# Optimization experiments

Hardware: AMD Instinct MI355X
Metric: run time of the kernel (lower is better)

## Reference

```python
import jax, jax.numpy as jnp
import numpy as np

B, T, E, H = 2, 2048, 1024, 16
D = E // H  # head_dim = 64


def setup_inputs() -> dict:
    key = jax.random.key(0)
    ks = jax.random.split(key, 9)
    s = 0.02
    x = jax.random.normal(ks[0], (B, T, E), dtype=jnp.float32)
    # additive causal mask, broadcastable to (B, H, T, T)
    causal = jnp.tril(jnp.ones((T, T), dtype=bool))
    uni_causal_mask = jnp.where(causal, 0.0, -1e9).astype(jnp.float32)[None, None]
    # torch Linear weights are (out_features, in_features); out = H*D, in = D
    Wq = jax.random.normal(ks[1], (H * D, D), dtype=jnp.float32) * s
    bq = jax.random.normal(ks[2], (H * D,), dtype=jnp.float32) * s
    Wk = jax.random.normal(ks[3], (H * D, D), dtype=jnp.float32) * s
    bk = jax.random.normal(ks[4], (H * D,), dtype=jnp.float32) * s
    Wv = jax.random.normal(ks[5], (H * D, D), dtype=jnp.float32) * s
    bv = jax.random.normal(ks[6], (H * D,), dtype=jnp.float32) * s
    Wp = jax.random.normal(ks[7], (E, E), dtype=jnp.float32) * s
    bp = jax.random.normal(ks[8], (E,), dtype=jnp.float32) * s
    return {"x": x, "uni_causal_mask": uni_causal_mask,
            "Wq": Wq, "bq": bq, "Wk": Wk, "bk": bk,
            "Wv": Wv, "bv": bv, "Wp": Wp, "bp": bp}


def _per_head_proj(xh, W, b):
    # xh: (B, T, H, D). Original code projects each head's D-dim slice with
    # Linear(D, H*D) and get_head_dim keeps only the diagonal block i for
    # head i, i.e. each head uses W[i*D:(i+1)*D, :] and b[i*D:(i+1)*D].
    W3 = W.reshape(H, D, D)  # (H, out D, in D)
    b2 = b.reshape(H, D)
    y = jnp.einsum('bthi,hoi->bhto', xh, W3) + b2[None, :, None, :]
    return y  # (B, H, T, D)


def reference(x, uni_causal_mask, Wq, bq, Wk, bk, Wv, bv, Wp, bp):
    b, t, e = x.shape
    xh = x.reshape(b, t, H, D)
    q = _per_head_proj(xh, Wq, bq)  # (B,H,T,D)
    k = _per_head_proj(xh, Wk, bk)
    v = _per_head_proj(xh, Wv, bv)
    scale = D ** (-0.5)
    attn = jnp.einsum('bhtd,bhsd->bhts', (q * scale).astype(jnp.float32),
                      k.astype(jnp.float32))
    attn = attn + uni_causal_mask
    attn = jax.nn.softmax(attn, axis=-1).astype(x.dtype)
    out = jnp.einsum('bhts,bhsd->bhtd', attn, v)
    out = out.transpose(0, 2, 1, 3).reshape(b, t, e)
    return out @ Wp.T + bp
```

## Files before the change

kernel.cpp:

```cpp
#include <hip/hip_runtime.h>

typedef __attribute__((ext_vector_type(4))) float f32x4;
typedef __attribute__((ext_vector_type(8))) __bf16 bf16x8;
typedef __attribute__((ext_vector_type(4))) unsigned short us4;
typedef __attribute__((ext_vector_type(8))) unsigned short us8;

#define DEVI static __device__ __forceinline__

constexpr int T_ = 2048, E_ = 1024, H_ = 16, D_ = 64;
#define QSCALE (0.125f * 1.44269504088896f)

DEVI unsigned short f2b(float f) {
  union { float fv; unsigned u; } c; c.fv = f;
  unsigned r = c.u + 0x7fffu + ((c.u >> 16) & 1u);
  return (unsigned short)(r >> 16);
}

#if __has_builtin(__builtin_amdgcn_exp2f)
DEVI float fexp2(float x) { return __builtin_amdgcn_exp2f(x); }
#else
DEVI float fexp2(float x) { return __expf(x * 0.69314718056f); }
#endif

DEVI f32x4 mfma16(bf16x8 a, bf16x8 b, f32x4 c) {
  return __builtin_amdgcn_mfma_f32_16x16x32_bf16(a, b, c, 0, 0, 0);
}

__launch_bounds__(256)
__global__ void wcvt_kernel(const float* __restrict__ Wq,
                            const float* __restrict__ Wk,
                            const float* __restrict__ Wv,
                            unsigned short* __restrict__ wqb,
                            unsigned short* __restrict__ wkb,
                            unsigned short* __restrict__ wvb)
{
  int blk = blockIdx.x;
  const float* src; unsigned short* dst; float s = 1.0f;
  if (blk < 64)       { src = Wq; dst = wqb; s = QSCALE; }
  else if (blk < 128) { src = Wk; dst = wkb; blk -= 64; }
  else                { src = Wv; dst = wvb; blk -= 128; }
  int i = blk * 256 + threadIdx.x;
  float4 v = *(const float4*)(src + (size_t)i * 4);
  us4 o; o[0] = f2b(v.x * s); o[1] = f2b(v.y * s); o[2] = f2b(v.z * s); o[3] = f2b(v.w * s);
  *(us4*)(dst + (size_t)i * 4) = o;
}

__launch_bounds__(256)
__global__ void wpcvt_kernel(const float* __restrict__ Wp,
                             unsigned short* __restrict__ wpb)
{
  int i = blockIdx.x * 256 + threadIdx.x;
  float4 v = *(const float4*)(Wp + (size_t)i * 4);
  us4 o; o[0] = f2b(v.x); o[1] = f2b(v.y); o[2] = f2b(v.z); o[3] = f2b(v.w);
  *(us4*)(wpb + (size_t)i * 4) = o;
}

__launch_bounds__(256)
__global__ void qkv_kernel(const float* __restrict__ x,
                           const unsigned short* __restrict__ wqb,
                           const float* __restrict__ bq,
                           const unsigned short* __restrict__ wkb,
                           const float* __restrict__ bk,
                           const unsigned short* __restrict__ wvb,
                           const float* __restrict__ bv,
                           unsigned short* __restrict__ qo,
                           unsigned short* __restrict__ ko,
                           unsigned short* __restrict__ vto)
{
  const int bh = blockIdx.x;
  const int b  = bh >> 4;
  const int h  = bh & (H_ - 1);
  const int t0 = blockIdx.y * 128;
  __shared__ unsigned short Xl[128][72];
  __shared__ unsigned short Wl[3][64][72];
  const int tid = threadIdx.x;

  #pragma unroll
  for (int p = 0; p < 8; ++p) {
    int idx = p * 256 + tid;
    int row = idx >> 4, c4 = idx & 15;
    const float* gp = x + ((size_t)(b * T_ + t0 + row)) * E_ + h * 64 + c4 * 4;
    float4 v = *(const float4*)gp;
    us4 o; o[0] = f2b(v.x); o[1] = f2b(v.y); o[2] = f2b(v.z); o[3] = f2b(v.w);
    *(us4*)&Xl[row][c4 * 4] = o;
  }
  {
    const unsigned short* wsrc0 = wqb + (size_t)h * 4096;
    const unsigned short* wsrc1 = wkb + (size_t)h * 4096;
    const unsigned short* wsrc2 = wvb + (size_t)h * 4096;
    #pragma unroll
    for (int p = 0; p < 2; ++p) {
      int idx = p * 256 + tid;
      int row = idx >> 3, c8 = (idx & 7) * 8;
      *(us8*)&Wl[0][row][c8] = *(const us8*)(wsrc0 + row * 64 + c8);
      *(us8*)&Wl[1][row][c8] = *(const us8*)(wsrc1 + row * 64 + c8);
      *(us8*)&Wl[2][row][c8] = *(const us8*)(wsrc2 + row * 64 + c8);
    }
  }
  __syncthreads();

  const int w = tid >> 6, lane = tid & 63, lo = lane & 15, g = lane >> 4;
  const int tl0 = w * 32;

  bf16x8 xb[2][2];
  #pragma unroll
  for (int tt = 0; tt < 2; ++tt)
    #pragma unroll
    for (int kd = 0; kd < 2; ++kd)
      xb[tt][kd] = *(const bf16x8*)&Xl[tl0 + tt * 16 + lo][kd * 32 + g * 8];

  #pragma unroll
  for (int tsel = 0; tsel < 2; ++tsel) {
    const float* bias = tsel ? bk : bq;
    unsigned short* outp = tsel ? ko : qo;
    const float bs = tsel ? 1.0f : QSCALE;
    #pragma unroll
    for (int ot = 0; ot < 4; ++ot) {
      bf16x8 a0 = *(const bf16x8*)&Wl[tsel][ot * 16 + lo][g * 8];
      bf16x8 a1 = *(const bf16x8*)&Wl[tsel][ot * 16 + lo][32 + g * 8];
      float4 bv4 = *(const float4*)(bias + h * 64 + ot * 16 + g * 4);
      float bb[4] = {bv4.x * bs, bv4.y * bs, bv4.z * bs, bv4.w * bs};
      #pragma unroll
      for (int tt = 0; tt < 2; ++tt) {
        f32x4 acc = {0.f, 0.f, 0.f, 0.f};
        acc = mfma16(a0, xb[tt][0], acc);
        acc = mfma16(a1, xb[tt][1], acc);
        int tg = t0 + tl0 + tt * 16 + lo;
        us4 pk;
        #pragma unroll
        for (int r = 0; r < 4; ++r) pk[r] = f2b(acc[r] + bb[r]);
        *(us4*)(outp + ((size_t)(bh * T_ + tg)) * 64 + ot * 16 + g * 4) = pk;
      }
    }
  }

  #pragma unroll
  for (int rt = 0; rt < 2; ++rt) {
    bf16x8 a0 = *(const bf16x8*)&Xl[tl0 + rt * 16 + lo][g * 8];
    bf16x8 a1 = *(const bf16x8*)&Xl[tl0 + rt * 16 + lo][32 + g * 8];
    #pragma unroll
    for (int ct = 0; ct < 4; ++ct) {
      bf16x8 b0 = *(const bf16x8*)&Wl[2][ct * 16 + lo][g * 8];
      bf16x8 b1 = *(const bf16x8*)&Wl[2][ct * 16 + lo][32 + g * 8];
      f32x4 acc = {0.f, 0.f, 0.f, 0.f};
      acc = mfma16(a0, b0, acc);
      acc = mfma16(a1, b1, acc);
      int d = ct * 16 + lo;
      float bvs = bv[h * 64 + d];
      int tg = t0 + tl0 + rt * 16 + g * 4;
      us4 pk;
      #pragma unroll
      for (int r = 0; r < 4; ++r) pk[r] = f2b(acc[r] + bvs);
      *(us4*)(vto + ((size_t)(bh * 64 + d)) * T_ + tg) = pk;
    }
  }
}

__launch_bounds__(256)
__global__ void flash_kernel(const unsigned short* __restrict__ q,
                             const unsigned short* __restrict__ kk_,
                             const unsigned short* __restrict__ vt,
                             unsigned short* __restrict__ ao)
{
  const int bh = blockIdx.x;
  const int b = bh >> 4, h = bh & 15;
  __shared__ unsigned short Kl[2][64][64];
  __shared__ unsigned short Vl[2][64][64];
  __shared__ unsigned short Pl[4][16][64];
  const int tid = threadIdx.x, w = tid >> 6, lane = tid & 63, lo = lane & 15, g = lane >> 4;
  const int rs = lo & 7;

  const int srow = tid >> 3, sgi = tid & 7;
  const int sgis = (sgi ^ (srow & 7)) * 8;
  const unsigned short* kbase = kk_ + ((size_t)bh * T_ + srow) * 64 + sgi * 8;
  const unsigned short* vbase = vt + ((size_t)(bh * 64 + srow)) * T_ + sgi * 8;

  #pragma unroll 1
  for (int half = 0; half < 2; ++half) {
    const int qt = half ? (31 - blockIdx.y) : blockIdx.y;
    const int t0 = qt * 64;
    const int tw = t0 + w * 16;

    bf16x8 qf[2];
    const unsigned short* qb = q + ((size_t)(bh * T_ + tw + lo)) * 64;
    #pragma unroll
    for (int kd = 0; kd < 2; ++kd)
      qf[kd] = *(const bf16x8*)(qb + kd * 32 + g * 8);

    float m_ = -1e30f, l_ = 0.f;
    f32x4 zero4 = {0.f, 0.f, 0.f, 0.f};
    f32x4 oacc[4];
    #pragma unroll
    for (int dt = 0; dt < 4; ++dt) oacc[dt] = zero4;

    const int nsteps = qt + 1;
    us8 kr0 = *(const us8*)(kbase);
    us8 kr1 = *(const us8*)(kbase + 2048);
    us8 vr0 = *(const us8*)(vbase);
    us8 vr1 = *(const us8*)(vbase + (size_t)32 * T_);
    *(us8*)&Kl[0][srow][sgis] = kr0;
    *(us8*)&Kl[0][srow + 32][sgis] = kr1;
    *(us8*)&Vl[0][srow][sgis] = vr0;
    *(us8*)&Vl[0][srow + 32][sgis] = vr1;
    if (nsteps > 1) {
      kr0 = *(const us8*)(kbase + 4096);
      kr1 = *(const us8*)(kbase + 4096 + 2048);
      vr0 = *(const us8*)(vbase + 64);
      vr1 = *(const us8*)(vbase + 64 + (size_t)32 * T_);
    }
    __syncthreads();

    for (int stp = 0; stp < nsteps; ++stp) {
      const int s0 = stp * 64;
      const int cur = stp & 1;
      us8 nk0, nk1, nv0, nv1;
      const bool pf = (stp + 2 < nsteps);
      if (pf) {
        const size_t ko_ = (size_t)(stp + 2) * 4096;
        nk0 = *(const us8*)(kbase + ko_);
        nk1 = *(const us8*)(kbase + ko_ + 2048);
        nv0 = *(const us8*)(vbase + (stp + 2) * 64);
        nv1 = *(const us8*)(vbase + (stp + 2) * 64 + (size_t)32 * T_);
      }
      {
        f32x4 sacc[4];
        #pragma unroll
        for (int ss = 0; ss < 4; ++ss) sacc[ss] = zero4;
        __builtin_amdgcn_s_setprio(1);
        #pragma unroll
        for (int ss = 0; ss < 4; ++ss) {
          bf16x8 ka0 = *(const bf16x8*)&Kl[cur][ss * 16 + lo][(g ^ rs) * 8];
          bf16x8 ka1 = *(const bf16x8*)&Kl[cur][ss * 16 + lo][((g | 4) ^ rs) * 8];
          sacc[ss] = mfma16(ka0, qf[0], sacc[ss]);
          sacc[ss] = mfma16(ka1, qf[1], sacc[ss]);
        }
        __builtin_amdgcn_s_setprio(0);
        if (s0 + 63 > tw) {
          #pragma unroll
          for (int ss = 0; ss < 4; ++ss)
            #pragma unroll
            for (int r = 0; r < 4; ++r) {
              int sg = s0 + ss * 16 + g * 4 + r;
              if (sg > tw + lo) sacc[ss][r] = -1e30f;
            }
        }
        float mx = -1e30f;
        #pragma unroll
        for (int ss = 0; ss < 4; ++ss)
          #pragma unroll
          for (int r = 0; r < 4; ++r) mx = fmaxf(mx, sacc[ss][r]);
        mx = fmaxf(mx, __shfl_xor(mx, 16));
        mx = fmaxf(mx, __shfl_xor(mx, 32));
        float mn = fmaxf(m_, mx);
        float corr = fexp2(m_ - mn);
        m_ = mn;
        float sum = 0.f;
        #pragma unroll
        for (int ss = 0; ss < 4; ++ss) {
          us4 pk;
          #pragma unroll
          for (int r = 0; r < 4; ++r) {
            float pv = fexp2(sacc[ss][r] - mn);
            sum += pv;
            pk[r] = f2b(pv);
          }
          *(us4*)&Pl[w][lo][(((ss * 2 + (g >> 1)) ^ rs) << 3) + (g & 1) * 4] = pk;
        }
        sum += __shfl_xor(sum, 16);
        sum += __shfl_xor(sum, 32);
        l_ = l_ * corr + sum;
        #pragma unroll
        for (int dt = 0; dt < 4; ++dt) oacc[dt] *= corr;
        __builtin_amdgcn_s_setprio(1);
        #pragma unroll
        for (int kh = 0; kh < 2; ++kh) {
          bf16x8 pb = *(const bf16x8*)&Pl[w][lo][((kh * 4 + g) ^ rs) * 8];
          #pragma unroll
          for (int dt = 0; dt < 4; ++dt) {
            bf16x8 va = *(const bf16x8*)&Vl[cur][dt * 16 + lo][((kh * 4 + g) ^ rs) * 8];
            oacc[dt] = mfma16(va, pb, oacc[dt]);
          }
        }
        __builtin_amdgcn_s_setprio(0);
      }
      if (stp + 1 < nsteps) {
        *(us8*)&Kl[cur ^ 1][srow][sgis] = kr0;
        *(us8*)&Kl[cur ^ 1][srow + 32][sgis] = kr1;
        *(us8*)&Vl[cur ^ 1][srow][sgis] = vr0;
        *(us8*)&Vl[cur ^ 1][srow + 32][sgis] = vr1;
      }
      __syncthreads();
      if (pf) { kr0 = nk0; kr1 = nk1; vr0 = nv0; vr1 = nv1; }
    }
    float inv = 1.0f / l_;
    unsigned short* op = ao + ((size_t)(b * T_ + tw + lo)) * E_ + h * 64;
    #pragma unroll
    for (int dt = 0; dt < 4; ++dt) {
      us4 pk;
      #pragma unroll
      for (int r = 0; r < 4; ++r) pk[r] = f2b(oacc[dt][r] * inv);
      *(us4*)(op + dt * 16 + g * 4) = pk;
    }
  }
}

__launch_bounds__(256)
__global__ void proj_kernel(const unsigned short* __restrict__ ao,
                            const unsigned short* __restrict__ wpb,
                            const float* __restrict__ bp,
                            float* __restrict__ out)
{
  const int m0 = blockIdx.x * 128;
  const int n0 = blockIdx.y * 64;
  __shared__ unsigned short Al[2][128][40];
  __shared__ unsigned short Bl[2][64][40];
  const int tid = threadIdx.x, w = tid >> 6, lane = tid & 63, lo = lane & 15, g = lane >> 4;
  const int wr = (w >> 1) * 64, wc = (w & 1) * 32;
  f32x4 zero4 = {0.f, 0.f, 0.f, 0.f};
  f32x4 acc[4][2];
  #pragma unroll
  for (int i = 0; i < 4; ++i)
    #pragma unroll
    for (int j = 0; j < 2; ++j) acc[i][j] = zero4;

  const int arow = tid >> 1, acol = (tid & 1) * 16;
  const int brow = tid >> 2, bcol = (tid & 3) * 8;
  const unsigned short* abase = ao + (size_t)(m0 + arow) * 1024 + acol;
  const unsigned short* bbase = wpb + (size_t)(n0 + brow) * 1024 + bcol;

  us8 a0 = *(const us8*)(abase);
  us8 a1 = *(const us8*)(abase + 8);
  us8 b0 = *(const us8*)(bbase);
  *(us8*)&Al[0][arow][acol] = a0;
  *(us8*)&Al[0][arow][acol + 8] = a1;
  *(us8*)&Bl[0][brow][bcol] = b0;
  a0 = *(const us8*)(abase + 32);
  a1 = *(const us8*)(abase + 40);
  b0 = *(const us8*)(bbase + 32);
  __syncthreads();

  for (int it = 0; it < 32; ++it) {
    const int cur = it & 1;
    us8 na0, na1, nb0;
    const bool pf = (it + 2 < 32);
    if (pf) {
      const int kn = (it + 2) * 32;
      na0 = *(const us8*)(abase + kn);
      na1 = *(const us8*)(abase + kn + 8);
      nb0 = *(const us8*)(bbase + kn);
    }
    bf16x8 af[4], bfr[2];
    #pragma unroll
    for (int i = 0; i < 4; ++i) af[i] = *(const bf16x8*)&Al[cur][wr + i * 16 + lo][g * 8];
    #pragma unroll
    for (int j = 0; j < 2; ++j) bfr[j] = *(const bf16x8*)&Bl[cur][wc + j * 16 + lo][g * 8];
    __builtin_amdgcn_s_setprio(1);
    #pragma unroll
    for (int i = 0; i < 4; ++i)
      #pragma unroll
      for (int j = 0; j < 2; ++j)
        acc[i][j] = mfma16(af[i], bfr[j], acc[i][j]);
    __builtin_amdgcn_s_setprio(0);
    if (it + 1 < 32) {
      *(us8*)&Al[cur ^ 1][arow][acol] = a0;
      *(us8*)&Al[cur ^ 1][arow][acol + 8] = a1;
      *(us8*)&Bl[cur ^ 1][brow][bcol] = b0;
    }
    __syncthreads();
    if (pf) { a0 = na0; a1 = na1; b0 = nb0; }
  }
  #pragma unroll
  for (int j = 0; j < 2; ++j) {
    int n = n0 + wc + j * 16 + lo;
    float bias = bp[n];
    #pragma unroll
    for (int i = 0; i < 4; ++i) {
      #pragma unroll
      for (int r = 0; r < 4; ++r)
        out[(size_t)(m0 + wr + i * 16 + g * 4 + r) * 1024 + n] = acc[i][j][r] + bias;
    }
  }
}

extern "C" void kernel_launch(void* const* d_in, const int* in_sizes, int n_in,
                              void* d_out, int out_size, void* d_ws, size_t ws_size,
                              hipStream_t stream)
{
  const float* x  = (const float*)d_in[0];
  const float* Wq = (const float*)d_in[2];
  const float* bq = (const float*)d_in[3];
  const float* Wk = (const float*)d_in[4];
  const float* bk = (const float*)d_in[5];
  const float* Wv = (const float*)d_in[6];
  const float* bv = (const float*)d_in[7];
  const float* Wp = (const float*)d_in[8];
  const float* bp = (const float*)d_in[9];
  float* out = (float*)d_out;

  char* ws = (char*)d_ws;
  const size_t SZ = (size_t)2 * 16 * 2048 * 64 * 2;
  unsigned short* q  = (unsigned short*)(ws);
  unsigned short* kb = (unsigned short*)(ws + SZ);
  unsigned short* vt = (unsigned short*)(ws + 2 * SZ);
  unsigned short* ao = (unsigned short*)(ws + 3 * SZ);
  unsigned short* wqb = ao;
  unsigned short* wkb = ao + 65536;
  unsigned short* wvb = ao + 131072;
  unsigned short* wpb = q;

  wcvt_kernel<<<dim3(192), 256, 0, stream>>>(Wq, Wk, Wv, wqb, wkb, wvb);
  qkv_kernel<<<dim3(32, 16), 256, 0, stream>>>(x, wqb, bq, wkb, bk, wvb, bv, q, kb, vt);
  flash_kernel<<<dim3(32, 16), 256, 0, stream>>>(q, kb, vt, ao);
  wpcvt_kernel<<<dim3(1024), 256, 0, stream>>>(Wp, wpb);
  proj_kernel<<<dim3(32, 16), 256, 0, stream>>>(ao, wpb, bp, out);
}
```

Measured before the change: 89.05 us.

## Restructure flash attention to 128-row query tiles with async LDS loads and lazy rescale

The flash kernel now gives each block one 128-row query tile, with every wave handling 32 rows. Each K/V tile loaded into LDS is therefore reused across twice as many query rows. Causal load balance is kept by pairing tiles through the blockIdx.y mapping. Register-staged K/V prefetch is replaced with direct global-to-LDS loads. The online-softmax rescale is skipped when the new row max exceeds the old by no more than 8, which keeps the output exact but lets the exp values grow larger. Separately, the QKV kernel moves to 64-row tiles with twice as many blocks, and the bf16 conversion uses the native cast. The costs are higher register pressure and a wave-uniform early-exit on the causal tile loop.

```diff
diff --git a/kernel.cpp b/kernel.cpp
--- a/kernel.cpp
+++ b/kernel.cpp
@@ -11,9 +11,7 @@
 #define QSCALE (0.125f * 1.44269504088896f)
 
 DEVI unsigned short f2b(float f) {
-  union { float fv; unsigned u; } c; c.fv = f;
-  unsigned r = c.u + 0x7fffu + ((c.u >> 16) & 1u);
-  return (unsigned short)(r >> 16);
+  union { __bf16 b; unsigned short u; } c; c.b = (__bf16)f; return c.u;
 }
 
 #if __has_builtin(__builtin_amdgcn_exp2f)
@@ -24,6 +22,12 @@
 
 DEVI f32x4 mfma16(bf16x8 a, bf16x8 b, f32x4 c) {
   return __builtin_amdgcn_mfma_f32_16x16x32_bf16(a, b, c, 0, 0, 0);
+}
+
+DEVI void gl16(const void* g, void* l) {
+  __builtin_amdgcn_global_load_lds(
+      (const __attribute__((address_space(1))) unsigned int*)g,
+      (__attribute__((address_space(3))) unsigned int*)l, 16, 0, 0);
 }
 
 __launch_bounds__(256)
@@ -70,17 +74,16 @@
   const int bh = blockIdx.x;
   const int b  = bh >> 4;
   const int h  = bh & (H_ - 1);
-  const int t0 = blockIdx.y * 128;
-  __shared__ unsigned short Xl[128][72];
+  const int t0 = blockIdx.y * 64;
+  __shared__ unsigned short Xl[64][72];
   __shared__ unsigned short Wl[3][64][72];
   const int tid = threadIdx.x;
 
   #pragma unroll
-  for (int p = 0; p < 8; ++p) {
+  for (int p = 0; p < 4; ++p) {
     int idx = p * 256 + tid;
     int row = idx >> 4, c4 = idx & 15;
-    const float* gp = x + ((size_t)(b * T_ + t0 + row)) * E_ + h * 64 + c4 * 4;
-    float4 v = *(const float4*)gp;
+    float4 v = *(const float4*)(x + ((size_t)(b * T_ + t0 + row)) * E_ + h * 64 + c4 * 4);
     us4 o; o[0] = f2b(v.x); o[1] = f2b(v.y); o[2] = f2b(v.z); o[3] = f2b(v.w);
     *(us4*)&Xl[row][c4 * 4] = o;
   }
@@ -100,14 +103,12 @@
   __syncthreads();
 
   const int w = tid >> 6, lane = tid & 63, lo = lane & 15, g = lane >> 4;
-  const int tl0 = w * 32;
-
-  bf16x8 xb[2][2];
-  #pragma unroll
-  for (int tt = 0; tt < 2; ++tt)
-    #pragma unroll
-    for (int kd = 0; kd < 2; ++kd)
-      xb[tt][kd] = *(const bf16x8*)&Xl[tl0 + tt * 16 + lo][kd * 32 + g * 8];
+  const int tl0 = w * 16;
+
+  bf16x8 xb[2];
+  #pragma unroll
+  for (int kd = 0; kd < 2; ++kd)
+    xb[kd] = *(const bf16x8*)&Xl[tl0 + lo][kd * 32 + g * 8];
 
   #pragma unroll
   for (int tsel = 0; tsel < 2; ++tsel) {
@@ -119,25 +120,20 @@
       bf16x8 a0 = *(const bf16x8*)&Wl[tsel][ot * 16 + lo][g * 8];
       bf16x8 a1 = *(const bf16x8*)&Wl[tsel][ot * 16 + lo][32 + g * 8];
       float4 bv4 = *(const float4*)(bias + h * 64 + ot * 16 + g * 4);
-      float bb[4] = {bv4.x * bs, bv4.y * bs, bv4.z * bs, bv4.w * bs};
-      #pragma unroll
-      for (int tt = 0; tt < 2; ++tt) {
-        f32x4 acc = {0.f, 0.f, 0.f, 0.f};
-        acc = mfma16(a0, xb[tt][0], acc);
-        acc = mfma16(a1, xb[tt][1], acc);
-        int tg = t0 + tl0 + tt * 16 + lo;
-        us4 pk;
-        #pragma unroll
-        for (int r = 0; r < 4; ++r) pk[r] = f2b(acc[r] + bb[r]);
-        *(us4*)(outp + ((size_t)(bh * T_ + tg)) * 64 + ot * 16 + g * 4) = pk;
-      }
-    }
-  }
-
-  #pragma unroll
-  for (int rt = 0; rt < 2; ++rt) {
-    bf16x8 a0 = *(const bf16x8*)&Xl[tl0 + rt * 16 + lo][g * 8];
-    bf16x8 a1 = *(const bf16x8*)&Xl[tl0 + rt * 16 + lo][32 + g * 8];
+      f32x4 acc = {0.f, 0.f, 0.f, 0.f};
+      acc = mfma16(a0, xb[0], acc);
+      acc = mfma16(a1, xb[1], acc);
+      int tg = t0 + tl0 + lo;
+      us4 pk;
+      pk[0] = f2b(acc[0] + bv4.x * bs); pk[1] = f2b(acc[1] + bv4.y * bs);
+      pk[2] = f2b(acc[2] + bv4.z * bs); pk[3] = f2b(acc[3] + bv4.w * bs);
+      *(us4*)(outp + ((size_t)(bh * T_ + tg)) * 64 + ot * 16 + g * 4) = pk;
+    }
+  }
+
+  {
+    bf16x8 a0 = *(const bf16x8*)&Xl[tl0 + lo][g * 8];
+    bf16x8 a1 = *(const bf16x8*)&Xl[tl0 + lo][32 + g * 8];
     #pragma unroll
     for (int ct = 0; ct < 4; ++ct) {
       bf16x8 b0 = *(const bf16x8*)&Wl[2][ct * 16 + lo][g * 8];
@@ -147,7 +143,7 @@
       acc = mfma16(a1, b1, acc);
       int d = ct * 16 + lo;
       float bvs = bv[h * 64 + d];
-      int tg = t0 + tl0 + rt * 16 + g * 4;
+      int tg = t0 + tl0 + g * 4;
       us4 pk;
       #pragma unroll
       for (int r = 0; r < 4; ++r) pk[r] = f2b(acc[r] + bvs);
@@ -164,141 +160,156 @@
 {
   const int bh = blockIdx.x;
   const int b = bh >> 4, h = bh & 15;
+  const int y = blockIdx.y;
+  const int qt = (y < 8) ? y : 23 - y;
+  const int t0 = qt * 128;
   __shared__ unsigned short Kl[2][64][64];
   __shared__ unsigned short Vl[2][64][64];
-  __shared__ unsigned short Pl[4][16][64];
+  __shared__ unsigned short Pl[4][32][64];
   const int tid = threadIdx.x, w = tid >> 6, lane = tid & 63, lo = lane & 15, g = lane >> 4;
   const int rs = lo & 7;
 
-  const int srow = tid >> 3, sgi = tid & 7;
-  const int sgis = (sgi ^ (srow & 7)) * 8;
-  const unsigned short* kbase = kk_ + ((size_t)bh * T_ + srow) * 64 + sgi * 8;
-  const unsigned short* vbase = vt + ((size_t)(bh * 64 + srow)) * T_ + sgi * 8;
-
-  #pragma unroll 1
-  for (int half = 0; half < 2; ++half) {
-    const int qt = half ? (31 - blockIdx.y) : blockIdx.y;
-    const int t0 = qt * 64;
-    const int tw = t0 + w * 16;
-
-    bf16x8 qf[2];
-    const unsigned short* qb = q + ((size_t)(bh * T_ + tw + lo)) * 64;
+  const int srow = tid >> 3, sgi = (tid & 7) ^ ((tid >> 3) & 7);
+  const unsigned short* kg0 = kk_ + ((size_t)bh * T_ + srow) * 64 + sgi * 8;
+  const unsigned short* kg1 = kg0 + 32 * 64;
+  const unsigned short* vg0 = vt + ((size_t)(bh * 64 + srow)) * T_ + sgi * 8;
+  const unsigned short* vg1 = vg0 + (size_t)32 * T_;
+
+  const int tw = t0 + w * 32;
+
+  bf16x8 qf[2][2];
+  const unsigned short* qb = q + ((size_t)(bh * T_ + tw)) * 64;
+  #pragma unroll
+  for (int tt = 0; tt < 2; ++tt)
     #pragma unroll
     for (int kd = 0; kd < 2; ++kd)
-      qf[kd] = *(const bf16x8*)(qb + kd * 32 + g * 8);
-
-    float m_ = -1e30f, l_ = 0.f;
-    f32x4 zero4 = {0.f, 0.f, 0.f, 0.f};
-    f32x4 oacc[4];
-    #pragma unroll
-    for (int dt = 0; dt < 4; ++dt) oacc[dt] = zero4;
-
-    const int nsteps = qt + 1;
-    us8 kr0 = *(const us8*)(kbase);
-    us8 kr1 = *(const us8*)(kbase + 2048);
-    us8 vr0 = *(const us8*)(vbase);
-    us8 vr1 = *(const us8*)(vbase + (size_t)32 * T_);
-    *(us8*)&Kl[0][srow][sgis] = kr0;
-    *(us8*)&Kl[0][srow + 32][sgis] = kr1;
-    *(us8*)&Vl[0][srow][sgis] = vr0;
-    *(us8*)&Vl[0][srow + 32][sgis] = vr1;
-    if (nsteps > 1) {
-      kr0 = *(const us8*)(kbase + 4096);
-      kr1 = *(const us8*)(kbase + 4096 + 2048);
-      vr0 = *(const us8*)(vbase + 64);
-      vr1 = *(const us8*)(vbase + 64 + (size_t)32 * T_);
-    }
-    __syncthreads();
-
-    for (int stp = 0; stp < nsteps; ++stp) {
-      const int s0 = stp * 64;
-      const int cur = stp & 1;
-      us8 nk0, nk1, nv0, nv1;
-      const bool pf = (stp + 2 < nsteps);
-      if (pf) {
-        const size_t ko_ = (size_t)(stp + 2) * 4096;
-        nk0 = *(const us8*)(kbase + ko_);
-        nk1 = *(const us8*)(kbase + ko_ + 2048);
-        nv0 = *(const us8*)(vbase + (stp + 2) * 64);
-        nv1 = *(const us8*)(vbase + (stp + 2) * 64 + (size_t)32 * T_);
-      }
-      {
-        f32x4 sacc[4];
-        #pragma unroll
-        for (int ss = 0; ss < 4; ++ss) sacc[ss] = zero4;
-        __builtin_amdgcn_s_setprio(1);
-        #pragma unroll
-        for (int ss = 0; ss < 4; ++ss) {
-          bf16x8 ka0 = *(const bf16x8*)&Kl[cur][ss * 16 + lo][(g ^ rs) * 8];
-          bf16x8 ka1 = *(const bf16x8*)&Kl[cur][ss * 16 + lo][((g | 4) ^ rs) * 8];
-          sacc[ss] = mfma16(ka0, qf[0], sacc[ss]);
-          sacc[ss] = mfma16(ka1, qf[1], sacc[ss]);
+      qf[tt][kd] = *(const bf16x8*)(qb + (size_t)(tt * 16 + lo) * 64 + kd * 32 + g * 8);
+
+  float m_[2] = {-1e30f, -1e30f};
+  float l_[2] = {0.f, 0.f};
+  f32x4 zero4 = {0.f, 0.f, 0.f, 0.f};
+  f32x4 oacc[4][2];
+  #pragma unroll
+  for (int dt = 0; dt < 4; ++dt)
+    #pragma unroll
+    for (int tt = 0; tt < 2; ++tt) oacc[dt][tt] = zero4;
+
+  const int nsteps = 2 * qt + 2;
+  gl16(kg0, &Kl[0][w * 8][0]);
+  gl16(kg1, &Kl[0][32 + w * 8][0]);
+  gl16(vg0, &Vl[0][w * 8][0]);
+  gl16(vg1, &Vl[0][32 + w * 8][0]);
+  __syncthreads();
+
+  for (int stp = 0; stp < nsteps; ++stp) {
+    const int s0 = stp * 64;
+    const int cur = stp & 1;
+    if (stp + 1 < nsteps) {
+      const int nb = cur ^ 1;
+      const size_t so = (size_t)(s0 + 64);
+      gl16(kg0 + so * 64, &Kl[nb][w * 8][0]);
+      gl16(kg1 + so * 64, &Kl[nb][32 + w * 8][0]);
+      gl16(vg0 + so, &Vl[nb][w * 8][0]);
+      gl16(vg1 + so, &Vl[nb][32 + w * 8][0]);
+    }
+    if (s0 <= tw + 31) {
+      f32x4 sacc[4][2];
+      #pragma unroll
+      for (int ss = 0; ss < 4; ++ss)
+        #pragma unroll
+        for (int tt = 0; tt < 2; ++tt) sacc[ss][tt] = zero4;
+      __builtin_amdgcn_s_setprio(1);
+      #pragma unroll
+      for (int ss = 0; ss < 4; ++ss) {
+        bf16x8 ka0 = *(const bf16x8*)&Kl[cur][ss * 16 + lo][(g ^ rs) * 8];
+        bf16x8 ka1 = *(const bf16x8*)&Kl[cur][ss * 16 + lo][((g | 4) ^ rs) * 8];
+        #pragma unroll
+        for (int tt = 0; tt < 2; ++tt) {
+          sacc[ss][tt] = mfma16(ka0, qf[tt][0], sacc[ss][tt]);
+          sacc[ss][tt] = mfma16(ka1, qf[tt][1], sacc[ss][tt]);
         }
-        __builtin_amdgcn_s_setprio(0);
-        if (s0 + 63 > tw) {
+      }
+      __builtin_amdgcn_s_setprio(0);
+      if (s0 + 63 > tw) {
+        #pragma unroll
+        for (int ss = 0; ss < 4; ++ss)
           #pragma unroll
-          for (int ss = 0; ss < 4; ++ss)
+          for (int tt = 0; tt < 2; ++tt)
             #pragma unroll
             for (int r = 0; r < 4; ++r) {
               int sg = s0 + ss * 16 + g * 4 + r;
-              if (sg > tw + lo) sacc[ss][r] = -1e30f;
+              if (sg > tw + tt * 16 + lo) sacc[ss][tt][r] = -1e30f;
             }
+      }
+      float mx[2];
+      #pragma unroll
+      for (int tt = 0; tt < 2; ++tt) {
+        float a = fmaxf(fmaxf(sacc[0][tt][0], sacc[0][tt][1]), fmaxf(sacc[0][tt][2], sacc[0][tt][3]));
+        float b2 = fmaxf(fmaxf(sacc[1][tt][0], sacc[1][tt][1]), fmaxf(sacc[1][tt][2], sacc[1][tt][3]));
+        float c = fmaxf(fmaxf(sacc[2][tt][0], sacc[2][tt][1]), fmaxf(sacc[2][tt][2], sacc[2][tt][3]));
+        float d = fmaxf(fmaxf(sacc[3][tt][0], sacc[3][tt][1]), fmaxf(sacc[3][tt][2], sacc[3][tt][3]));
+        float m = fmaxf(fmaxf(a, b2), fmaxf(c, d));
+        m = fmaxf(m, __shfl_xor(m, 16));
+        m = fmaxf(m, __shfl_xor(m, 32));
+        mx[tt] = m;
+      }
+      if (!__all((mx[0] <= m_[0] + 8.0f) && (mx[1] <= m_[1] + 8.0f))) {
+        #pragma unroll
+        for (int tt = 0; tt < 2; ++tt) {
+          float mn = fmaxf(m_[tt], mx[tt]);
+          float corr = fexp2(m_[tt] - mn);
+          m_[tt] = mn;
+          l_[tt] *= corr;
+          #pragma unroll
+          for (int dt = 0; dt < 4; ++dt) oacc[dt][tt] *= corr;
         }
-        float mx = -1e30f;
-        #pragma unroll
-        for (int ss = 0; ss < 4; ++ss)
-          #pragma unroll
-          for (int r = 0; r < 4; ++r) mx = fmaxf(mx, sacc[ss][r]);
-        mx = fmaxf(mx, __shfl_xor(mx, 16));
-        mx = fmaxf(mx, __shfl_xor(mx, 32));
-        float mn = fmaxf(m_, mx);
-        float corr = fexp2(m_ - mn);
-        m_ = mn;
+      }
+      #pragma unroll
+      for (int tt = 0; tt < 2; ++tt) {
         float sum = 0.f;
         #pragma unroll
         for (int ss = 0; ss < 4; ++ss) {
           us4 pk;
           #pragma unroll
           for (int r = 0; r < 4; ++r) {
-            float pv = fexp2(sacc[ss][r] - mn);
+            float pv = fexp2(sacc[ss][tt][r] - m_[tt]);
             sum += pv;
             pk[r] = f2b(pv);
           }
-          *(us4*)&Pl[w][lo][(((ss * 2 + (g >> 1)) ^ rs) << 3) + (g & 1) * 4] = pk;
+          *(us4*)&Pl[w][tt * 16 + lo][(((ss * 2 + (g >> 1)) ^ rs) << 3) + (g & 1) * 4] = pk;
         }
         sum += __shfl_xor(sum, 16);
         sum += __shfl_xor(sum, 32);
-        l_ = l_ * corr + sum;
-        #pragma unroll
-        for (int dt = 0; dt < 4; ++dt) oacc[dt] *= corr;
-        __builtin_amdgcn_s_setprio(1);
-        #pragma unroll
-        for (int kh = 0; kh < 2; ++kh) {
-          bf16x8 pb = *(const bf16x8*)&Pl[w][lo][((kh * 4 + g) ^ rs) * 8];
+        l_[tt] += sum;
+      }
+      __builtin_amdgcn_s_setprio(1);
+      #pragma unroll
+      for (int kh = 0; kh < 2; ++kh) {
+        bf16x8 pb[2];
+        #pragma unroll
+        for (int tt = 0; tt < 2; ++tt)
+          pb[tt] = *(const bf16x8*)&Pl[w][tt * 16 + lo][((kh * 4 + g) ^ rs) * 8];
+        #pragma unroll
+        for (int dt = 0; dt < 4; ++dt) {
+          bf16x8 va = *(const bf16x8*)&Vl[cur][dt * 16 + lo][((kh * 4 + g) ^ rs) * 8];
           #pragma unroll
-          for (int dt = 0; dt < 4; ++dt) {
-            bf16x8 va = *(const bf16x8*)&Vl[cur][dt * 16 + lo][((kh * 4 + g) ^ rs) * 8];
-            oacc[dt] = mfma16(va, pb, oacc[dt]);
-          }
+          for (int tt = 0; tt < 2; ++tt)
+            oacc[dt][tt] = mfma16(va, pb[tt], oacc[dt][tt]);
         }
-        __builtin_amdgcn_s_setprio(0);
-      }
-      if (stp + 1 < nsteps) {
-        *(us8*)&Kl[cur ^ 1][srow][sgis] = kr0;
-        *(us8*)&Kl[cur ^ 1][srow + 32][sgis] = kr1;
-        *(us8*)&Vl[cur ^ 1][srow][sgis] = vr0;
-        *(us8*)&Vl[cur ^ 1][srow + 32][sgis] = vr1;
-      }
-      __syncthreads();
-      if (pf) { kr0 = nk0; kr1 = nk1; vr0 = nv0; vr1 = nv1; }
-    }
-    float inv = 1.0f / l_;
-    unsigned short* op = ao + ((size_t)(b * T_ + tw + lo)) * E_ + h * 64;
+      }
+      __builtin_amdgcn_s_setprio(0);
+    }
+    __syncthreads();
+  }
+  #pragma unroll
+  for (int tt = 0; tt < 2; ++tt) {
+    float inv = 1.0f / l_[tt];
+    unsigned short* op = ao + ((size_t)(b * T_ + tw + tt * 16 + lo)) * E_ + h * 64;
     #pragma unroll
     for (int dt = 0; dt < 4; ++dt) {
       us4 pk;
       #pragma unroll
-      for (int r = 0; r < 4; ++r) pk[r] = f2b(oacc[dt][r] * inv);
+      for (int r = 0; r < 4; ++r) pk[r] = f2b(oacc[dt][tt][r] * inv);
       *(us4*)(op + dt * 16 + g * 4) = pk;
     }
   }
@@ -409,7 +420,7 @@
   unsigned short* wpb = q;
 
   wcvt_kernel<<<dim3(192), 256, 0, stream>>>(Wq, Wk, Wv, wqb, wkb, wvb);
-  qkv_kernel<<<dim3(32, 16), 256, 0, stream>>>(x, wqb, bq, wkb, bk, wvb, bv, q, kb, vt);
+  qkv_kernel<<<dim3(32, 32), 256, 0, stream>>>(x, wqb, bq, wkb, bk, wvb, bv, q, kb, vt);
   flash_kernel<<<dim3(32, 16), 256, 0, stream>>>(q, kb, vt, ao);
   wpcvt_kernel<<<dim3(1024), 256, 0, stream>>>(Wp, wpb);
   proj_kernel<<<dim3(32, 16), 256, 0, stream>>>(ao, wpb, bp, out);
```

New measurement: 97.50 us. +9.5%, slower.
